# Performance work log

Measured on AMD Instinct MI355X. Metric: run time of the kernel, lower is better.

The kernel has to match this reference:

```python
import jax, jax.numpy as jnp
import numpy as np
from jax.scipy.special import gammaln

REG = 0.1  # reg_param from __init__


def setup_inputs() -> dict:
    key = jax.random.key(0)
    k1, k2 = jax.random.split(key)
    D, C, S, Q = 512, 64, 16, 2048  # feature_dim, n_way, shots, n_query
    X_support = jax.random.normal(k1, (C * S, D), dtype=jnp.float32)
    # balanced class labels (equivalent to argmax of a one-hot y)
    labels = jnp.arange(C * S, dtype=jnp.int32) % C
    X_query = jax.random.normal(k2, (Q, D), dtype=jnp.float32)
    # learned parameters, initialized exactly as in the torch module
    m = jnp.zeros((1, D), dtype=jnp.float32)
    kappa = jnp.asarray(0.1, dtype=jnp.float32)
    nu = jnp.asarray(float(D), dtype=jnp.float32)
    triu_diag = jnp.ones((D,), dtype=jnp.float32)
    triu_lower = jnp.eye(D, dtype=jnp.float32)
    return {"X_support": X_support, "labels": labels, "X_query": X_query,
            "m": m, "kappa": kappa, "nu": nu,
            "triu_diag": triu_diag, "triu_lower": triu_lower, "n_classes": 64}


def _forward(X_support, X_query, m, kappa, nu, triu_diag, triu_lower, labels, n_classes):
    N, D = X_support.shape
    C = int(n_classes)
    S = N // C  # balanced episode: N_j == S for every class

    # lower_triu = diag(|triu_diag|) + triu_lower * strictly_lower_mask
    mask = jnp.tril(jnp.ones((D, D), dtype=X_support.dtype), -1)
    L = jnp.diag(jnp.abs(triu_diag)) + triu_lower * mask

    kap = jnp.abs(kappa) + 1e-6
    nu_ = jnp.clip(nu, D - 1 + 1e-6)

    # group support samples by class: [C, S, D] (stable sort keeps per-class order)
    order = jnp.argsort(labels)
    Xg = X_support[order].reshape(C, S, D)
    Xmean = Xg.mean(axis=1)  # [C, D]

    # posterior means mu_j = kappa/(kappa+N) m + N/(kappa+N) mean(X_j)
    mu = (kap / (kap + S)) * m + (S / (kap + S)) * Xmean  # [C, D]

    # sum_outer(X_j) as one batched GEMM instead of a per-row loop
    XtX = jnp.einsum('csd,cse->cde', Xg, Xg)  # [C, D, D]
    base = L @ L.T + kap * (m.T @ m)          # [D, D], shared across classes
    S_ns = base[None] + XtX - (kap + S) * jnp.einsum('cd,ce->cde', mu, mu)
    sigma = S_ns * ((kap + S + 1.0) / ((nu_ + S - D + 1.0) * (kap + S)))  # [C, D, D]

    eye = jnp.eye(D, dtype=sigma.dtype)
    sigma_inv = (1.0 - REG) * jnp.linalg.inv(sigma) + REG * eye  # regularize()

    common = nu_ + S + 1.0 - D  # scalar (equal shots per class)
    _, logdet = jnp.linalg.slogdet(sigma)  # [C]
    bias = (gammaln(0.5 * (common + D)) - gammaln(0.5 * common)
            - 0.5 * D * jnp.log(common) - 0.5 * logdet)  # [C]

    # batched Mahalanobis distances: replaces nested python loops in predict()
    diff = X_query[None, :, :] - mu[:, None, :]              # [C, Q, D]
    t = jnp.einsum('cqd,cde->cqe', diff, sigma_inv)          # [C, Q, D]
    dist = jnp.sum(t * diff, axis=-1)                        # [C, Q]

    logits = bias[:, None] - 0.5 * (common + D) * jnp.log1p(dist / common)
    return logits.T  # [Q, C]


def reference(X_support, labels, X_query, m, kappa, nu, triu_diag, triu_lower, n_classes):
    return _forward(X_support, X_query, m, kappa, nu, triu_diag, triu_lower,
                    labels, n_classes)
```

## Files before the change

### kernel.cpp

```cpp
#include <hip/hip_runtime.h>
#include <math.h>

#define DD    512
#define CNUM  64
#define SHOTS 16
#define NSUP  1024
#define QNQ   2048
#define REGP  0.1f
#define XKS   4

typedef __attribute__((ext_vector_type(8))) short short8;
typedef __attribute__((ext_vector_type(4))) float f32x4;

__device__ __forceinline__ unsigned short f2bf(float f) {
  unsigned int u = __float_as_uint(f);
  unsigned int r = (u + 0x7fffu + ((u >> 16) & 1u)) >> 16;
  return (unsigned short)r;
}
__device__ __forceinline__ float bf2f(unsigned short h) {
  return __uint_as_float((unsigned int)h << 16);
}

static constexpr size_t OFF_W     = 0;
static constexpr size_t OFF_MU    = OFF_W     + 512*512;
static constexpr size_t OFF_Y     = OFF_MU    + 64*512;
static constexpr size_t OFF_Z     = OFF_Y     + 3136*512;
static constexpr size_t OFF_WM    = OFF_Z     + 3136;
static constexpr size_t OFF_CONST = OFF_WM    + 512;
static constexpr size_t OFF_IDX   = OFF_CONST + 16;
static constexpr size_t OFF_RMAP  = OFF_IDX   + 1024;
static constexpr size_t OFF_ZG    = OFF_RMAP  + 1088;
static constexpr size_t OFF_VMU   = OFF_ZG    + 1088;
static constexpr size_t OFF_MUBMU = OFF_VMU   + 1088;
static constexpr size_t OFF_MUN   = OFF_MUBMU + 64;
static constexpr size_t OFF_MINV  = OFF_MUN   + 64;
static constexpr size_t OFF_BIAS  = OFF_MINV  + 64*289;
static constexpr size_t OFF_QNRM  = OFF_BIAS  + 64;
static constexpr size_t OFF_YN    = OFF_QNRM  + 2048;
static constexpr size_t OFF_XMU   = OFF_YN    + 2048;
static constexpr size_t OFF_RG    = OFF_XMU   + (size_t)XKS*2048*64;
static constexpr size_t OFF_P     = OFF_RG    + 1088*2048;
static constexpr size_t OFF_PX    = OFF_P     + 3136*512;
static constexpr size_t OFF_PW    = OFF_PX    + 3136*512;


__global__ __launch_bounds__(256) void f_init(const float* tdiag, const float* tlow,
    const float* kappa, const float* nu, const int* labels, const float* Xs,
    const float* Xq, const float* m, float* W, float* cst, int* idx,
    int* rowmap, float* mu, float* mun,
    unsigned short* PX, unsigned short* PW) {
  __shared__ float sh[2 * 64 * 68 + 32 * 33];
  __shared__ int sidx[SHOTS];
  int b = blockIdx.x, tid = threadIdx.x;
  if (b == 0) {
    if (tid == 0) {
      float kap = fabsf(kappa[0]) + 1e-6f;
      float nu_ = fmaxf(nu[0], (float)(DD - 1) + 1e-6f);
      float common = nu_ + (float)SHOTS + 1.0f - (float)DD;
      float scale = (kap + SHOTS + 1.0f) / ((nu_ + SHOTS - DD + 1.0f) * (kap + SHOTS));
      cst[0] = kap;
      cst[1] = scale;
      cst[2] = common;
      cst[3] = 0.5f * (common + DD);
      cst[4] = lgammaf(0.5f * (common + DD)) - lgammaf(0.5f * common)
               - 0.5f * (float)DD * logf(common);
      cst[5] = -(kap + SHOTS);
      cst[6] = kap / (kap + SHOTS);
      cst[7] = 1.0f / (kap + SHOTS);
      cst[8] = (float)DD * logf(scale);
      cst[9] = -1.0f / (kap + SHOTS);
    }
  } else if (b < 65) {
    int c = b - 1;
    if (tid < 64) {
      int lane = tid, cnt = 0;
      for (int i0 = 0; i0 < NSUP; i0 += 64) {
        int lab = labels[i0 + lane];
        unsigned long long mm = __ballot(lab == c);
        if (lab == c) {
          int pos = cnt + __popcll(mm & ((1ull << lane) - 1ull));
          if (pos < SHOTS) idx[c * SHOTS + pos] = i0 + lane;
        }
        cnt += __popcll(mm);
      }
    }
    __syncthreads();
    if (tid < 17)
      rowmap[c * 17 + tid] = (tid < SHOTS) ? (QNQ + idx[c * SHOTS + tid])
                                           : (QNQ + NSUP + c);
  } else if (b < 129) {
    int c = b - 65;
    if (tid < 64) {
      int lane = tid, cnt = 0;
      for (int i0 = 0; i0 < NSUP; i0 += 64) {
        int lab = labels[i0 + lane];
        unsigned long long mm = __ballot(lab == c);
        if (lab == c) {
          int pos = cnt + __popcll(mm & ((1ull << lane) - 1ull));
          if (pos < SHOTS) sidx[pos] = i0 + lane;
        }
        cnt += __popcll(mm);
      }
    }
    __syncthreads();
    float kap = fabsf(kappa[0]) + 1e-6f;
    float cm = kap / (kap + SHOTS), cx = 1.0f / (kap + SHOTS);
    float* red = sh;
    float acc = 0.0f;
    size_t prow = (size_t)(3072 + c) * 1024;
    for (int d = tid; d < DD; d += 256) {
      float s = 0.0f;
      for (int sh_ = 0; sh_ < SHOTS; sh_++)
        s += Xs[(size_t)sidx[sh_] * DD + d];
      float v = cm * m[d] + cx * s;
      mu[(size_t)c * DD + d] = v;
      unsigned short h = f2bf(v), l = f2bf(v - bf2f(h));
      PX[prow + d] = h;
      PX[prow + 512 + d] = l;
      acc += v * v;
    }
    red[tid] = acc;
    __syncthreads();
    for (int off = 128; off > 0; off >>= 1) {
      if (tid < off) red[tid] += red[tid + off];
      __syncthreads();
    }
    if (tid == 0) mun[c] = red[0];
  } else if (b < 137) {
    int jb = b - 129;
    float* Ld = sh;
    float* Wd = sh + 64 * 68;
    float* tsh = sh + 2 * 64 * 68;
    for (int t = tid; t < 4096; t += 256) {
      int r = t >> 6, c = t & 63;
      int gr = jb * 64 + r;
      float v = (r == c) ? fabsf(tdiag[gr])
              : (r > c ? tlow[(size_t)gr * DD + jb * 64 + c] : 0.0f);
      Ld[r * 68 + c] = v;
      Wd[r * 68 + c] = 0.0f;
    }
    __syncthreads();
    if (tid < 64) {
      int s = tid >> 4, t = tid & 15;
      int r0 = s * 16;
      #pragma unroll
      for (int i = 0; i < 16; i++) {
        float w = (i == t) ? 1.0f : 0.0f;
        #pragma unroll
        for (int k = 0; k < 16; k++)
          if (k < i) w -= Ld[(r0 + i) * 68 + r0 + k] * Wd[(r0 + k) * 68 + r0 + t];
        Wd[(r0 + i) * 68 + r0 + t] = w / Ld[(r0 + i) * 68 + r0 + i];
      }
    }
    __syncthreads();
    for (int g2 = 0; g2 < 2; g2++) {
      int r0 = g2 * 32 + 16, c0 = g2 * 32;
      int rr = tid >> 4, cc = tid & 15;
      float t_ = 0.0f;
      #pragma unroll
      for (int k = 0; k < 16; k++)
        t_ += Ld[(r0 + rr) * 68 + c0 + k] * Wd[(c0 + k) * 68 + c0 + cc];
      tsh[rr * 33 + cc] = t_;
      __syncthreads();
      float x = 0.0f;
      #pragma unroll
      for (int k = 0; k < 16; k++)
        x -= Wd[(r0 + rr) * 68 + r0 + k] * tsh[k * 33 + cc];
      Wd[(r0 + rr) * 68 + c0 + cc] = x;
      __syncthreads();
    }
    {
      int rr = tid >> 6, cc = tid & 63;
      #pragma unroll
      for (int p = 0; p < 4; p++) {
        int r = rr + p * 4, c = cc;
        if (c < 32) {
          float t_ = 0.0f;
          #pragma unroll
          for (int k = 0; k < 32; k++)
            t_ += Ld[(32 + r) * 68 + k] * Wd[k * 68 + c];
          tsh[r * 33 + c] = t_;
        } else {
          int c2 = c - 32;
          float t_ = 0.0f;
          #pragma unroll
          for (int k = 0; k < 32; k++)
            t_ += Ld[(32 + r + 16) * 68 + k] * Wd[k * 68 + c2];
          tsh[(r + 16) * 33 + c2] = t_;
        }
      }
      __syncthreads();
      #pragma unroll
      for (int p = 0; p < 4; p++) {
        int r = rr + p * 4, c = cc;
        int r2 = (c < 32) ? r : r + 16;
        int c2 = (c < 32) ? c : c - 32;
        float x = 0.0f;
        #pragma unroll
        for (int k = 0; k < 32; k++)
          x -= Wd[(32 + r2) * 68 + 32 + k] * tsh[k * 33 + c2];
        Wd[(32 + r2) * 68 + c2] = x;
      }
    }
    __syncthreads();
    float* Wblk = W + (size_t)(jb * 64) * DD + jb * 64;
    for (int t = tid; t < 4096; t += 256) {
      int r = t >> 6, c = t & 63;
      float v = Wd[r * 68 + c];
      Wblk[(size_t)r * DD + c] = v;
      unsigned short h = f2bf(v), l = f2bf(v - bf2f(h));
      size_t prow = (size_t)(jb * 64 + r) * 1024 + jb * 64 + c;
      PW[prow] = h;
      PW[prow + 512] = l;
    }
  } else {
    int r0 = (b - 137) * 4;
    int row = r0 + (tid >> 6), lane = tid & 63;
    const float* src = (row < QNQ) ? Xq + (size_t)row * DD
                                   : Xs + (size_t)(row - QNQ) * DD;
    size_t prow = (size_t)row * 1024;
    #pragma unroll
    for (int p = 0; p < 2; p++) {
      int col = lane * 8 + p * 4;
      float4 v = *(const float4*)(src + col);
      ushort4 hi, lo;
      hi.x = f2bf(v.x); lo.x = f2bf(v.x - bf2f(hi.x));
      hi.y = f2bf(v.y); lo.y = f2bf(v.y - bf2f(hi.y));
      hi.z = f2bf(v.z); lo.z = f2bf(v.z - bf2f(hi.z));
      hi.w = f2bf(v.w); lo.w = f2bf(v.w - bf2f(hi.w));
      *(ushort4*)(PX + prow + col) = hi;
      *(ushort4*)(PX + prow + 512 + col) = lo;
    }
  }
}

__device__ __forceinline__ void tile_stage(float* S, const float* __restrict__ G, int ldg) {
  int tid = threadIdx.x;
  #pragma unroll
  for (int p = 0; p < 4; p++) {
    int f4 = tid + 256 * p;
    int row = f4 >> 4, c4 = (f4 & 15) * 4;
    *(float4*)&S[row * 68 + c4] = *(const float4*)(G + (size_t)row * ldg + c4);
  }
}
__device__ __forceinline__ void tile_fma(float acc[4][4], const float* As, const float* Bs) {
  int tid = threadIdx.x, tr = tid >> 4, tc = tid & 15;
  #pragma unroll
  for (int kk = 0; kk < 64; kk++) {
    float a[4];
    #pragma unroll
    for (int x = 0; x < 4; x++) a[x] = As[(tr * 4 + x) * 68 + kk];
    float4 bv = *(const float4*)&Bs[kk * 68 + tc * 4];
    float bb[4] = {bv.x, bv.y, bv.z, bv.w};
    #pragma unroll
    for (int x = 0; x < 4; x++)
      #pragma unroll
      for (int y = 0; y < 4; y++) acc[x][y] += a[x] * bb[y];
  }
}
__device__ __forceinline__ void tile_out_neg(const float acc[4][4], float* W,
    unsigned short* PW, int gr0, int gc0) {
  int tid = threadIdx.x, tr = tid >> 4, tc = tid & 15;
  #pragma unroll
  for (int x = 0; x < 4; x++) {
    #pragma unroll
    for (int y = 0; y < 4; y++) {
      float v = -acc[x][y];
      W[(size_t)(gr0 + tr * 4 + x) * DD + gc0 + tc * 4 + y] = v;
      unsigned short h = f2bf(v), l = f2bf(v - bf2f(h));
      size_t prow = (size_t)(gr0 + tr * 4 + x) * 1024 + gc0 + tc * 4 + y;
      PW[prow] = h;
      PW[prow + 512] = l;
    }
  }
}

#define GBK 16
__global__ __launch_bounds__(256) void k_m128_xmu(const float* __restrict__ tlow,
    const float* __restrict__ W_, float* __restrict__ Wout,
    const float* __restrict__ Xq, const float* __restrict__ Mu,
    float* __restrict__ xmup, unsigned short* __restrict__ PW) {
  __shared__ float sh[3 * 64 * 68];
  int b = blockIdx.x, tid = threadIdx.x;
  if (b < 4) {
    float* As = sh;
    float* Bs = sh + 64 * 68;
    float* tsh = sh + 2 * 64 * 68;
    int base = b * 128;
    float tacc[4][4] = {};
    tile_stage(As, tlow + (size_t)(base + 64) * DD + base, DD);
    tile_stage(Bs, W_ + (size_t)base * DD + base, DD);
    __syncthreads();
    tile_fma(tacc, As, Bs);
    __syncthreads();
    {
      int tr = tid >> 4, tc = tid & 15;
      #pragma unroll
      for (int x = 0; x < 4; x++)
        #pragma unroll
        for (int y = 0; y < 4; y++) tsh[(tr * 4 + x) * 68 + tc * 4 + y] = tacc[x][y];
    }
    tile_stage(As, W_ + (size_t)(base + 64) * DD + base + 64, DD);
    __syncthreads();
    float xacc[4][4] = {};
    tile_fma(xacc, As, tsh);
    tile_out_neg(xacc, Wout, PW, base + 64, base);
  } else {
    float* Ms = sh;
    float* Qs = sh + 64 * 68;
    int xb = b - 4;
    int bm = (xb & 63) * 32, kq = xb >> 6;
    int tr = tid >> 4, tc = tid & 15;
    float acc[4][2] = {};
    int k0s = kq * (DD / XKS), k0e = k0s + DD / XKS;
    for (int k0 = k0s; k0 < k0e; k0 += GBK) {
      {
        int row = tid >> 2, k4 = tid & 3;
        float4 v = *(const float4*)(Mu + (size_t)row * DD + k0 + k4 * 4);
        Ms[(k4 * 4 + 0) * 68 + row] = v.x; Ms[(k4 * 4 + 1) * 68 + row] = v.y;
        Ms[(k4 * 4 + 2) * 68 + row] = v.z; Ms[(k4 * 4 + 3) * 68 + row] = v.w;
      }
      if (tid < 128) {
        int row = tid >> 2, k4 = tid & 3;
        float4 v = *(const float4*)(Xq + (size_t)(bm + row) * DD + k0 + k4 * 4);
        Qs[(k4 * 4 + 0) * 36 + row] = v.x; Qs[(k4 * 4 + 1) * 36 + row] = v.y;
        Qs[(k4 * 4 + 2) * 36 + row] = v.z; Qs[(k4 * 4 + 3) * 36 + row] = v.w;
      }
      __syncthreads();
      #pragma unroll
      for (int kk = 0; kk < GBK; kk++) {
        float4 m0 = *(const float4*)&Ms[kk * 68 + tr * 4];
        float a[4] = {m0.x, m0.y, m0.z, m0.w};
        float q0 = Qs[kk * 36 + tc * 2], q1 = Qs[kk * 36 + tc * 2 + 1];
        #pragma unroll
        for (int y = 0; y < 4; y++) {
          acc[y][0] += a[y] * q0;
          acc[y][1] += a[y] * q1;
        }
      }
      __syncthreads();
    }
    #pragma unroll
    for (int y = 0; y < 4; y++) {
      float2 v = make_float2(acc[y][0], acc[y][1]);
      *(float2*)(xmup + ((size_t)kq * CNUM + tr * 4 + y) * QNQ + bm + tc * 2) = v;
    }
  }
}

__global__ __launch_bounds__(256) void k_m256(const float* __restrict__ tlow,
    float* __restrict__ W, unsigned short* __restrict__ PW) {
  __shared__ float sh[3 * 64 * 68];
  float* As = sh;
  float* Bs = sh + 64 * 68;
  float* tsh = sh + 2 * 64 * 68;
  int b = blockIdx.x, tid = threadIdx.x;
  int g = b >> 2, rem = b & 3, i = rem >> 1, j = rem & 1;
  int base = g * 256;
  float xacc[4][4] = {};
  for (int k = 0; k <= i; k++) {
    float tacc[4][4] = {};
    for (int l = j; l < 2; l++) {
      __syncthreads();
      tile_stage(As, tlow + (size_t)(base + 128 + 64 * k) * DD + base + 64 * l, DD);
      tile_stage(Bs, W + (size_t)(base + 64 * l) * DD + base + 64 * j, DD);
      __syncthreads();
      tile_fma(tacc, As, Bs);
    }
    __syncthreads();
    {
      int tr = tid >> 4, tc = tid & 15;
      #pragma unroll
      for (int x = 0; x < 4; x++)
        #pragma unroll
        for (int y = 0; y < 4; y++) tsh[(tr * 4 + x) * 68 + tc * 4 + y] = tacc[x][y];
    }
    tile_stage(As, W + (size_t)(base + 128 + 64 * i) * DD + base + 128 + 64 * k, DD);
    __syncthreads();
    tile_fma(xacc, As, tsh);
  }
  tile_out_neg(xacc, W, PW, base + 128 + 64 * i, base + 64 * j);
}

__device__ __forceinline__ void nn64_sh(float* As, float* Bs,
    const float* __restrict__ A, int lda, const float* __restrict__ B, int ldb,
    float* __restrict__ Cd, int ldc, int k0, int k1, float sgn,
    unsigned short* __restrict__ Pw, int gr0, int gc0) {
  int tid = threadIdx.x, tr = tid >> 4, tc = tid & 15;
  float acc[4][4] = {};
  for (int kc = k0; kc < k1; kc += 64) {
    #pragma unroll
    for (int p = 0; p < 4; p++) {
      int f4 = tid + 256 * p;
      int row = f4 >> 4, c4 = f4 & 15;
      *(float4*)&As[row * 68 + c4 * 4] = *(const float4*)(A + (size_t)row * lda + kc + c4 * 4);
      *(float4*)&Bs[row * 68 + c4 * 4] = *(const float4*)(B + (size_t)(kc + row) * ldb + c4 * 4);
    }
    __syncthreads();
    #pragma unroll
    for (int kk = 0; kk < 64; kk++) {
      float a[4];
      #pragma unroll
      for (int x = 0; x < 4; x++) a[x] = As[(tr * 4 + x) * 68 + kk];
      float4 bv = *(const float4*)&Bs[kk * 68 + tc * 4];
      float bb[4] = {bv.x, bv.y, bv.z, bv.w};
      #pragma unroll
      for (int x = 0; x < 4; x++)
        #pragma unroll
        for (int y = 0; y < 4; y++) acc[x][y] += a[x] * bb[y];
    }
    __syncthreads();
  }
  #pragma unroll
  for (int x = 0; x < 4; x++) {
    float4 v = make_float4(sgn * acc[x][0], sgn * acc[x][1],
                           sgn * acc[x][2], sgn * acc[x][3]);
    *(float4*)(Cd + (size_t)(tr * 4 + x) * ldc + tc * 4) = v;
    if (Pw) {
      size_t prow = (size_t)(gr0 + tr * 4 + x) * 1024 + gc0 + tc * 4;
      float vv[4] = {v.x, v.y, v.z, v.w};
      #pragma unroll
      for (int y = 0; y < 4; y++) {
        unsigned short h = f2bf(vv[y]), l = f2bf(vv[y] - bf2f(h));
        Pw[prow + y] = h;
        Pw[prow + 512 + y] = l;
      }
    }
  }
}

__global__ __launch_bounds__(256) void k_triT(const float* __restrict__ tlow,
                                              const float* __restrict__ W,
                                              float* __restrict__ T, int s) {
  __shared__ float sh[2 * 64 * 68];
  int h = s >> 1, tiles = h >> 6, per = tiles * tiles;
  int g = blockIdx.x / per, rem = blockIdx.x % per;
  int ti = rem / tiles, tj = rem % tiles;
  int base = g * s;
  const float* A = tlow + (size_t)(base + h + ti * 64) * DD + base;
  const float* B = W + (size_t)base * DD + base + tj * 64;
  float* Cd = T + (size_t)g * h * h + (size_t)(ti * 64) * h + tj * 64;
  nn64_sh(sh, sh + 64 * 68, A, DD, B, DD, Cd, h, tj * 64, h, 1.0f, nullptr, 0, 0);
}

__global__ __launch_bounds__(256) void k_triX(float* __restrict__ W,
                                              const float* __restrict__ T, int s,
                                              unsigned short* __restrict__ PW) {
  __shared__ float sh[2 * 64 * 68];
  int h = s >> 1, tiles = h >> 6, per = tiles * tiles;
  int g = blockIdx.x / per, rem = blockIdx.x % per;
  int ti = rem / tiles, tj = rem % tiles;
  int base = g * s;
  const float* A = W + (size_t)(base + h + ti * 64) * DD + base + h;
  const float* B = T + (size_t)g * h * h + tj * 64;
  int gr0 = base + h + ti * 64, gc0 = base + tj * 64;
  float* Cd = W + (size_t)gr0 * DD + gc0;
  nn64_sh(sh, sh + 64 * 68, A, DD, B, h, Cd, DD, 0, (ti + 1) * 64, -1.0f, PW, gr0, gc0);
}

#define PSTR 80
__global__ __launch_bounds__(256) void f_y_wm(const unsigned short* __restrict__ PX,
    const unsigned short* __restrict__ PW, const float* __restrict__ W,
    const float* __restrict__ m, float* __restrict__ Y,
    unsigned short* __restrict__ Pm, float* __restrict__ wm) {
  __shared__ unsigned short AshH[64 * PSTR];
  __shared__ unsigned short AshL[64 * PSTR];
  __shared__ unsigned short BshH[64 * PSTR];
  __shared__ unsigned short BshL[64 * PSTR];
  int b = blockIdx.x, tid = threadIdx.x;
  if (b < 392) {
    int mt = b >> 3, nt = b & 7;
    int bm = mt * 64, bn = nt * 64;
    int lane = tid & 63, wave = tid >> 6;
    int wr = wave >> 1, wc = wave & 1;
    int mrow = lane & 15, q = lane >> 4;
    f32x4 acc00 = {}, acc01 = {}, acc10 = {}, acc11 = {};
    int kchunks = nt + 1;
    for (int it = 0; it < kchunks; it++) {
      int kc = it * 64;
      #pragma unroll
      for (int p = 0; p < 2; p++) {
        int idx = tid + 256 * p;
        int row = idx >> 3, c8 = (idx & 7) * 8;
        *(short8*)&AshH[row * PSTR + c8] =
            *(const short8*)(PX + (size_t)(bm + row) * 1024 + kc + c8);
        *(short8*)&AshL[row * PSTR + c8] =
            *(const short8*)(PX + (size_t)(bm + row) * 1024 + 512 + kc + c8);
        *(short8*)&BshH[row * PSTR + c8] =
            *(const short8*)(PW + (size_t)(bn + row) * 1024 + kc + c8);
        *(short8*)&BshL[row * PSTR + c8] =
            *(const short8*)(PW + (size_t)(bn + row) * 1024 + 512 + kc + c8);
      }
      __syncthreads();
      #pragma unroll
      for (int ks = 0; ks < 2; ks++) {
        int ko = ks * 32 + q * 8;
        short8 ah0 = *(const short8*)&AshH[(wr * 32 + mrow) * PSTR + ko];
        short8 ah1 = *(const short8*)&AshH[(wr * 32 + 16 + mrow) * PSTR + ko];
        short8 al0 = *(const short8*)&AshL[(wr * 32 + mrow) * PSTR + ko];
        short8 al1 = *(const short8*)&AshL[(wr * 32 + 16 + mrow) * PSTR + ko];
        short8 bh0 = *(const short8*)&BshH[(wc * 32 + mrow) * PSTR + ko];
        short8 bh1 = *(const short8*)&BshH[(wc * 32 + 16 + mrow) * PSTR + ko];
        short8 bl0 = *(const short8*)&BshL[(wc * 32 + mrow) * PSTR + ko];
        short8 bl1 = *(const short8*)&BshL[(wc * 32 + 16 + mrow) * PSTR + ko];
        acc00 = __builtin_amdgcn_mfma_f32_16x16x32_bf16(ah0, bh0, acc00, 0, 0, 0);
        acc00 = __builtin_amdgcn_mfma_f32_16x16x32_bf16(ah0, bl0, acc00, 0, 0, 0);
        acc00 = __builtin_amdgcn_mfma_f32_16x16x32_bf16(al0, bh0, acc00, 0, 0, 0);
        acc00 = __builtin_amdgcn_mfma_f32_16x16x32_bf16(al0, bl0, acc00, 0, 0, 0);
        acc01 = __builtin_amdgcn_mfma_f32_16x16x32_bf16(ah0, bh1, acc01, 0, 0, 0);
        acc01 = __builtin_amdgcn_mfma_f32_16x16x32_bf16(ah0, bl1, acc01, 0, 0, 0);
        acc01 = __builtin_amdgcn_mfma_f32_16x16x32_bf16(al0, bh1, acc01, 0, 0, 0);
        acc01 = __builtin_amdgcn_mfma_f32_16x16x32_bf16(al0, bl1, acc01, 0, 0, 0);
        acc10 = __builtin_amdgcn_mfma_f32_16x16x32_bf16(ah1, bh0, acc10, 0, 0, 0);
        acc10 = __builtin_amdgcn_mfma_f32_16x16x32_bf16(ah1, bl0, acc10, 0, 0, 0);
        acc10 = __builtin_amdgcn_mfma_f32_16x16x32_bf16(al1, bh0, acc10, 0, 0, 0);
        acc10 = __builtin_amdgcn_mfma_f32_16x16x32_bf16(al1, bl0, acc10, 0, 0, 0);
        acc11 = __builtin_amdgcn_mfma_f32_16x16x32_bf16(ah1, bh1, acc11, 0, 0, 0);
        acc11 = __builtin_amdgcn_mfma_f32_16x16x32_bf16(ah1, bl1, acc11, 0, 0, 0);
        acc11 = __builtin_amdgcn_mfma_f32_16x16x32_bf16(al1, bh1, acc11, 0, 0, 0);
        acc11 = __builtin_amdgcn_mfma_f32_16x16x32_bf16(al1, bl1, acc11, 0, 0, 0);
      }
      __syncthreads();
    }
    #pragma unroll
    for (int r = 0; r < 4; r++) {
      int row0 = bm + wr * 32 + q * 4 + r;
      int row1 = row0 + 16;
      int col0 = bn + wc * 32 + mrow;
      float vv[4] = {acc00[r], acc01[r], acc10[r], acc11[r]};
      int rows[4] = {row0, row0, row1, row1};
      int cols[4] = {col0, col0 + 16, col0, col0 + 16};
      #pragma unroll
      for (int e = 0; e < 4; e++) {
        Y[(size_t)rows[e] * DD + cols[e]] = vv[e];
        unsigned short h = f2bf(vv[e]), l = f2bf(vv[e] - bf2f(h));
        Pm[(size_t)rows[e] * 1024 + cols[e]] = h;
        Pm[(size_t)rows[e] * 1024 + 512 + cols[e]] = l;
      }
    }
  } else {
    int wave = tid >> 6, lane = tid & 63;
    int row = (b - 392) * 4 + wave;
    float s = 0.0f;
    for (int j = lane; j <= row; j += 64) s += W[(size_t)row * DD + j] * m[j];
    for (int off = 32; off > 0; off >>= 1) s += __shfl_down(s, off);
    if (lane == 0) wm[row] = s;
  }
}

__global__ __launch_bounds__(256) void f_z_rg_gram(const unsigned short* __restrict__ Pm,
    const float* __restrict__ Y, const float* __restrict__ tdiag,
    const int* __restrict__ rowmap, const float* __restrict__ Xq,
    const float* __restrict__ wm, float* __restrict__ cst,
    float* __restrict__ Rg,
    float* __restrict__ z, float* __restrict__ qn, float* __restrict__ yn,
    float* __restrict__ zg, float* __restrict__ Vmu, float* __restrict__ muBmu,
    float* __restrict__ Minv, float* __restrict__ bias) {
  __shared__ float sh[9920];
  __shared__ float csmS;
  int b = blockIdx.x, tid = threadIdx.x;
  if (b < 64) {
    int c = b;
    int lane = tid & 63, wave = tid >> 6;
    float* Ys  = sh;
    float* aug = sh + 8772;
    float* zsv = aug + 306;
    float kap = cst[0], cst9 = cst[9];
    for (int t = tid; t < 17 * 128; t += 256) {
      int r = t >> 7, col = t & 127;
      *(float4*)&Ys[r * 516 + col * 4] =
          *(const float4*)(Y + (size_t)rowmap[c * 17 + r] * DD + col * 4);
    }
    float ldb_r = 0.0f;
    if (wave == 0) {
      float aa = 0.0f, ll = 0.0f;
      for (int t = lane; t < DD; t += 64) {
        float w = wm[t]; aa += w * w;
        ll += logf(fabsf(tdiag[t]));
      }
      #pragma unroll
      for (int off = 32; off > 0; off >>= 1) {
        aa += __shfl_xor(aa, off);
        ll += __shfl_xor(ll, off);
      }
      ldb_r = 2.0f * ll + logf(1.0f + kap * aa);
      if (lane == 0) csmS = kap / (1.0f + kap * aa);
    }
    __syncthreads();
    if (wave > 0) {
      for (int a = wave - 1; a < 17; a += 3) {
        float s = 0.0f;
        for (int j = lane; j < 128; j += 64) {
          float4 yv = *(const float4*)&Ys[a * 516 + j * 4];
          float4 wv = *(const float4*)(wm + j * 4);
          s += yv.x * wv.x + yv.y * wv.y + yv.z * wv.z + yv.w * wv.w;
        }
        #pragma unroll
        for (int off = 32; off > 0; off >>= 1) s += __shfl_xor(s, off);
        if (lane == 0) zsv[a] = s;
      }
    }
    __syncthreads();
    float csm = csmS;
    for (int e = tid; e < 153; e += 256) {
      int a = (int)((sqrtf(8.0f * (float)e + 1.0f) - 1.0f) * 0.5f);
      while (((a + 1) * (a + 2)) / 2 <= e) a++;
      while ((a * (a + 1)) / 2 > e) a--;
      int bb = e - (a * (a + 1)) / 2;
      const float* ra = &Ys[a * 516];
      const float* rb = &Ys[bb * 516];
      float s = 0.0f;
      for (int k = 0; k < 128; k++) {
        float4 va = *(const float4*)&ra[k * 4];
        float4 vb = *(const float4*)&rb[k * 4];
        s += va.x * vb.x + va.y * vb.y + va.z * vb.z + va.w * vb.w;
      }
      float g = s - csm * zsv[a] * zsv[bb];
      if (a == bb) g += (a < 16) ? 1.0f : cst9;
      aug[a * 18 + bb] = g;
      if (a != bb) aug[bb * 18 + a] = g;
    }
    __syncthreads();
    if (wave == 0) {
      float colv[17];
      bool left = lane < 17;
      bool right = (lane >= 17 && lane < 34);
      #pragma unroll
      for (int r = 0; r < 17; r++) {
        float lv = aug[r * 18 + (lane & 31)];
        colv[r] = left ? lv : ((right && (lane - 17) == r) ? 1.0f : 0.0f);
      }
      float det = 0.0f;
      #pragma unroll
      for (int k = 0; k < 17; k++) {
        float best = fabsf(colv[k]); int bp = k;
        #pragma unroll
        for (int r = k + 1; r < 17; r++) {
          float v = fabsf(colv[r]);
          if (v > best) { best = v; bp = r; }
        }
        int p = __shfl(bp, k);
        float pv = colv[k];
        #pragma unroll
        for (int r = k + 1; r < 17; r++) pv = (p == r) ? colv[r] : pv;
        float oldk = colv[k];
        #pragma unroll
        for (int r = k + 1; r < 17; r++) colv[r] = (p == r) ? oldk : colv[r];
        colv[k] = pv;
        float piv = __shfl(pv, k);
        if (lane == 0) det += logf(fabsf(piv));
        float invp = 1.0f / piv;
        float rk = pv * invp;
        colv[k] = rk;
        #pragma unroll
        for (int r = 0; r < 17; r++) {
          if (r == k) continue;
          float ck = __shfl(colv[r], k);
          colv[r] = fmaf(-ck, rk, colv[r]);
        }
      }
      if (right) {
        int bb = lane - 17;
        #pragma unroll
        for (int r = 0; r < 17; r++)
          Minv[(size_t)c * 289 + r * 17 + bb] = colv[r];
      }
      if (lane == 0) {
        float slog = logf(fabsf(cst[5])) + det;
        float logdetSigma = cst[8] + ldb_r + slog;
        bias[c] = cst[4] - 0.5f * logdetSigma;
      }
    } else if (wave == 1) {
      if (lane < 17) {
        float gv = aug[lane * 18 + 16];
        if (lane == 16) gv -= cst9;
        Vmu[c * 17 + lane] = gv;
        if (lane == 16) muBmu[c] = gv;
        zg[c * 17 + lane] = zsv[lane];
      }
    }
  } else if (b == 64) {
    if (tid < 64) {
      float aa = 0.0f, ll = 0.0f;
      for (int t = tid; t < DD; t += 64) {
        float w = wm[t]; aa += w * w;
        ll += logf(fabsf(tdiag[t]));
      }
      #pragma unroll
      for (int off = 32; off > 0; off >>= 1) {
        aa += __shfl_xor(aa, off);
        ll += __shfl_xor(ll, off);
      }
      if (tid == 0) {
        float kap = cst[0];
        cst[10] = kap / (1.0f + kap * aa);
        cst[11] = 2.0f * ll + logf(1.0f + kap * aa);
      }
    }
  } else if (b < 609) {
    unsigned short* ush = (unsigned short*)sh;
    unsigned short* Ash = ush;
    unsigned short* Bsh = ush + 64 * PSTR;
    unsigned short* Csh = ush + 2 * 64 * PSTR;
    int rb = b - 65;
    int bm = (rb >> 5) * 64, bn = (rb & 31) * 64;
    int lane = tid & 63, wave = tid >> 6;
    int wr = wave >> 1, wc = wave & 1;
    int mrow = lane & 15, q = lane >> 4;
    int srowA[2];
    #pragma unroll
    for (int p = 0; p < 2; p++) srowA[p] = rowmap[bm + ((tid + 256 * p) >> 3)];
    f32x4 acc00 = {}, acc01 = {}, acc10 = {}, acc11 = {};
    for (int it = 0; it < 16; it++) {
      int kc = it * 64;
      int kcX = kc ^ 512;
      #pragma unroll
      for (int p = 0; p < 2; p++) {
        int idx = tid + 256 * p;
        int row = idx >> 3, c8 = (idx & 7) * 8;
        *(short8*)&Ash[row * PSTR + c8] =
            *(const short8*)(Pm + (size_t)srowA[p] * 1024 + kc + c8);
        *(short8*)&Bsh[row * PSTR + c8] =
            *(const short8*)(Pm + (size_t)(bn + row) * 1024 + kc + c8);
        *(short8*)&Csh[row * PSTR + c8] =
            *(const short8*)(Pm + (size_t)(bn + row) * 1024 + kcX + c8);
      }
      __syncthreads();
      #pragma unroll
      for (int ks = 0; ks < 2; ks++) {
        int ko = ks * 32 + q * 8;
        short8 a0 = *(const short8*)&Ash[(wr * 32 + mrow) * PSTR + ko];
        short8 a1 = *(const short8*)&Ash[(wr * 32 + 16 + mrow) * PSTR + ko];
        short8 b0 = *(const short8*)&Bsh[(wc * 32 + mrow) * PSTR + ko];
        short8 b1 = *(const short8*)&Bsh[(wc * 32 + 16 + mrow) * PSTR + ko];
        short8 c0 = *(const short8*)&Csh[(wc * 32 + mrow) * PSTR + ko];
        short8 c1 = *(const short8*)&Csh[(wc * 32 + 16 + mrow) * PSTR + ko];
        acc00 = __builtin_amdgcn_mfma_f32_16x16x32_bf16(a0, b0, acc00, 0, 0, 0);
        acc01 = __builtin_amdgcn_mfma_f32_16x16x32_bf16(a0, b1, acc01, 0, 0, 0);
        acc10 = __builtin_amdgcn_mfma_f32_16x16x32_bf16(a1, b0, acc10, 0, 0, 0);
        acc11 = __builtin_amdgcn_mfma_f32_16x16x32_bf16(a1, b1, acc11, 0, 0, 0);
        acc00 = __builtin_amdgcn_mfma_f32_16x16x32_bf16(a0, c0, acc00, 0, 0, 0);
        acc01 = __builtin_amdgcn_mfma_f32_16x16x32_bf16(a0, c1, acc01, 0, 0, 0);
        acc10 = __builtin_amdgcn_mfma_f32_16x16x32_bf16(a1, c0, acc10, 0, 0, 0);
        acc11 = __builtin_amdgcn_mfma_f32_16x16x32_bf16(a1, c1, acc11, 0, 0, 0);
      }
      __syncthreads();
    }
    #pragma unroll
    for (int r = 0; r < 4; r++) {
      int row0 = bm + wr * 32 + q * 4 + r;
      int row1 = row0 + 16;
      int col0 = bn + wc * 32 + mrow;
      Rg[(size_t)row0 * QNQ + col0]      = acc00[r];
      Rg[(size_t)row0 * QNQ + col0 + 16] = acc01[r];
      Rg[(size_t)row1 * QNQ + col0]      = acc10[r];
      Rg[(size_t)row1 * QNQ + col0 + 16] = acc11[r];
    }
  } else {
    int wave = tid >> 6, lane = tid & 63;
    int row = (b - 609) * 4 + wave;
    const float* xr = Xq + (size_t)row * DD;
    const float* yr = Y + (size_t)row * DD;
    float sz = 0.0f, s1 = 0.0f, s2 = 0.0f;
    for (int j4 = lane; j4 < 128; j4 += 64) {
      float4 xv = *(const float4*)(xr + j4 * 4);
      float4 yv = *(const float4*)(yr + j4 * 4);
      float4 wv = *(const float4*)(wm + j4 * 4);
      sz += yv.x * wv.x + yv.y * wv.y + yv.z * wv.z + yv.w * wv.w;
      s1 += xv.x * xv.x + xv.y * xv.y + xv.z * xv.z + xv.w * xv.w;
      s2 += yv.x * yv.x + yv.y * yv.y + yv.z * yv.z + yv.w * yv.w;
    }
    for (int off = 32; off > 0; off >>= 1) {
      sz += __shfl_down(sz, off);
      s1 += __shfl_down(s1, off);
      s2 += __shfl_down(s2, off);
    }
    if (lane == 0) {
      z[row] = sz;
      qn[row] = s1;
      yn[row] = s2;
    }
  }
}

__global__ __launch_bounds__(256) void k_logits(const float* __restrict__ Rg,
    const float* z, const float* zg,
    const float* Vmu, const float* muBmu, const float* mun, const float* yn,
    const float* qn, const float* xmup, const float* Minv, const float* bias,
    const float* cst, float* out) {
  __shared__ float Ms[289], Vs[17], Zs[17];
  int c = blockIdx.y;
  int q = blockIdx.x * 256 + threadIdx.x;
  for (int t = threadIdx.x; t < 289; t += 256) Ms[t] = Minv[(size_t)c * 289 + t];
  if (threadIdx.x < 17) {
    Vs[threadIdx.x] = Vmu[c * 17 + threadIdx.x];
    Zs[threadIdx.x] = zg[c * 17 + threadIdx.x];
  }
  __syncthreads();
  float csm = cst[10], scale = cst[1], common = cst[2], coef = cst[3];
  float zq = z[q];
  float r[17];
  float xBmu = 0.0f;
  for (int a = 0; a < 17; a++) {
    float raw = Rg[(size_t)(c * 17 + a) * QNQ + q] - csm * Zs[a] * zq;
    if (a == 16) xBmu = raw;
    r[a] = raw - Vs[a];
  }
  float qB = yn[q] - csm * zq * zq;
  float quadB = qB - 2.0f * xBmu + muBmu[c];
  float corr = 0.0f;
  for (int a = 0; a < 17; a++) {
    float e = 0.0f;
    for (int bb = 0; bb < 17; bb++) e += Ms[a * 17 + bb] * r[bb];
    corr += r[a] * e;
  }
  float distB = (quadB - corr) / scale;
  float xm = 0.0f;
  #pragma unroll
  for (int p = 0; p < XKS; p++)
    xm += xmup[((size_t)(p * CNUM + c)) * QNQ + q];
  float dn = qn[q] - 2.0f * xm + mun[c];
  float dist = (1.0f - REGP) * distB + REGP * dn;
  out[(size_t)q * CNUM + c] = bias[c] - coef * log1pf(dist / common);
}

extern "C" void kernel_launch(void* const* d_in, const int* in_sizes, int n_in,
                              void* d_out, int out_size, void* d_ws, size_t ws_size,
                              hipStream_t stream) {
  const float* Xs    = (const float*)d_in[0];
  const int*   labels= (const int*)d_in[1];
  const float* Xq    = (const float*)d_in[2];
  const float* m     = (const float*)d_in[3];
  const float* kappa = (const float*)d_in[4];
  const float* nu    = (const float*)d_in[5];
  const float* tdiag = (const float*)d_in[6];
  const float* tlow  = (const float*)d_in[7];
  float* ws = (float*)d_ws;
  float* W    = ws + OFF_W;
  float* mu   = ws + OFF_MU;
  float* Y    = ws + OFF_Y;
  float* z    = ws + OFF_Z;
  float* wm   = ws + OFF_WM;
  float* cst  = ws + OFF_CONST;
  int*   idx  = (int*)(ws + OFF_IDX);
  int*   rmap = (int*)(ws + OFF_RMAP);
  float* zg   = ws + OFF_ZG;
  float* Vmu  = ws + OFF_VMU;
  float* muBmu= ws + OFF_MUBMU;
  float* mun  = ws + OFF_MUN;
  float* Minv = ws + OFF_MINV;
  float* bias = ws + OFF_BIAS;
  float* qn   = ws + OFF_QNRM;
  float* yn   = ws + OFF_YN;
  float* xmup = ws + OFF_XMU;
  float* Rg   = ws + OFF_RG;
  unsigned short* P  = (unsigned short*)(ws + OFF_P);
  unsigned short* PX = (unsigned short*)(ws + OFF_PX);
  unsigned short* PW = (unsigned short*)(ws + OFF_PW);
  float* Ttmp = ws + OFF_RG;
  float* out  = (float*)d_out;

  f_init<<<905, 256, 0, stream>>>(tdiag, tlow, kappa, nu, labels, Xs, Xq, m,
                                  W, cst, idx, rmap, mu, mun, PX, PW);
  k_m128_xmu<<<260, 256, 0, stream>>>(tlow, W, W, Xq, mu, xmup, PW);
  k_m256<<<8, 256, 0, stream>>>(tlow, W, PW);
  k_triT<<<16, 256, 0, stream>>>(tlow, W, Ttmp, 512);
  k_triX<<<16, 256, 0, stream>>>(W, Ttmp, 512, PW);
  f_y_wm<<<520, 256, 0, stream>>>(PX, PW, W, m, Y, P, wm);
  f_z_rg_gram<<<64 + 1 + 544 + 512, 256, 0, stream>>>(P, Y, tdiag, rmap, Xq, wm,
                                                      cst, Rg, z, qn, yn,
                                                      zg, Vmu, muBmu, Minv, bias);
  k_logits<<<dim3(QNQ / 256, CNUM), 256, 0, stream>>>(Rg, z, zg, Vmu, muBmu,
                                                      mun, yn, qn, xmup, Minv, bias,
                                                      cst, out);
  (void)in_sizes; (void)n_in; (void)out_size; (void)ws_size;
}
```

Measured before the change: 189.1 us.

## Spread bf16 split conversion across small kernels and drop lo*lo MFMA terms

Moves the fp32-to-bf16 hi/lo split of query and support rows out of the init kernel into spare blocks of the under-occupied triangular-solve kernels, so that work fills otherwise idle CUs. The triangular-solve blocks move to the front of the init grid so the slowest blocks start first. Both split-bf16 GEMMs now skip the low*low product, the gram GEMM is restructured from a K=1024 swapped-half loop to an explicit hi/lo 3-term loop, and the LDS padding stride is reduced. Dropping the lo*lo term slightly lowers precision.

```diff
diff --git a/kernel.cpp b/kernel.cpp
--- a/kernel.cpp
+++ b/kernel.cpp
@@ -44,6 +44,27 @@
 static constexpr size_t OFF_PW    = OFF_PX    + 3136*512;
 
 
+__device__ __forceinline__ void px_rows(const float* __restrict__ Xq,
+    const float* __restrict__ Xs, unsigned short* __restrict__ PX, int r0) {
+  int tid = threadIdx.x;
+  int row = r0 + (tid >> 6), lane = tid & 63;
+  const float* src = (row < QNQ) ? Xq + (size_t)row * DD
+                                 : Xs + (size_t)(row - QNQ) * DD;
+  size_t prow = (size_t)row * 1024;
+  #pragma unroll
+  for (int p = 0; p < 2; p++) {
+    int col = lane * 8 + p * 4;
+    float4 v = *(const float4*)(src + col);
+    ushort4 hi, lo;
+    hi.x = f2bf(v.x); lo.x = f2bf(v.x - bf2f(hi.x));
+    hi.y = f2bf(v.y); lo.y = f2bf(v.y - bf2f(hi.y));
+    hi.z = f2bf(v.z); lo.z = f2bf(v.z - bf2f(hi.z));
+    hi.w = f2bf(v.w); lo.w = f2bf(v.w - bf2f(hi.w));
+    *(ushort4*)(PX + prow + col) = hi;
+    *(ushort4*)(PX + prow + 512 + col) = lo;
+  }
+}
+
 __global__ __launch_bounds__(256) void f_init(const float* tdiag, const float* tlow,
     const float* kappa, const float* nu, const int* labels, const float* Xs,
     const float* Xq, const float* m, float* W, float* cst, int* idx,
@@ -52,7 +73,94 @@
   __shared__ float sh[2 * 64 * 68 + 32 * 33];
   __shared__ int sidx[SHOTS];
   int b = blockIdx.x, tid = threadIdx.x;
-  if (b == 0) {
+  if (b < 8) {
+    int jb = b;
+    float* Ld = sh;
+    float* Wd = sh + 64 * 68;
+    float* tsh = sh + 2 * 64 * 68;
+    for (int t = tid; t < 4096; t += 256) {
+      int r = t >> 6, c = t & 63;
+      int gr = jb * 64 + r;
+      float v = (r == c) ? fabsf(tdiag[gr])
+              : (r > c ? tlow[(size_t)gr * DD + jb * 64 + c] : 0.0f);
+      Ld[r * 68 + c] = v;
+      Wd[r * 68 + c] = 0.0f;
+    }
+    __syncthreads();
+    if (tid < 64) {
+      int s = tid >> 4, t = tid & 15;
+      int r0 = s * 16;
+      #pragma unroll
+      for (int i = 0; i < 16; i++) {
+        float w = (i == t) ? 1.0f : 0.0f;
+        #pragma unroll
+        for (int k = 0; k < 16; k++)
+          if (k < i) w -= Ld[(r0 + i) * 68 + r0 + k] * Wd[(r0 + k) * 68 + r0 + t];
+        Wd[(r0 + i) * 68 + r0 + t] = w / Ld[(r0 + i) * 68 + r0 + i];
+      }
+    }
+    __syncthreads();
+    for (int g2 = 0; g2 < 2; g2++) {
+      int r0 = g2 * 32 + 16, c0 = g2 * 32;
+      int rr = tid >> 4, cc = tid & 15;
+      float t_ = 0.0f;
+      #pragma unroll
+      for (int k = 0; k < 16; k++)
+        t_ += Ld[(r0 + rr) * 68 + c0 + k] * Wd[(c0 + k) * 68 + c0 + cc];
+      tsh[rr * 33 + cc] = t_;
+      __syncthreads();
+      float x = 0.0f;
+      #pragma unroll
+      for (int k = 0; k < 16; k++)
+        x -= Wd[(r0 + rr) * 68 + r0 + k] * tsh[k * 33 + cc];
+      Wd[(r0 + rr) * 68 + c0 + cc] = x;
+      __syncthreads();
+    }
+    {
+      int rr = tid >> 6, cc = tid & 63;
+      #pragma unroll
+      for (int p = 0; p < 4; p++) {
+        int r = rr + p * 4, c = cc;
+        if (c < 32) {
+          float t_ = 0.0f;
+          #pragma unroll
+          for (int k = 0; k < 32; k++)
+            t_ += Ld[(32 + r) * 68 + k] * Wd[k * 68 + c];
+          tsh[r * 33 + c] = t_;
+        } else {
+          int c2 = c - 32;
+          float t_ = 0.0f;
+          #pragma unroll
+          for (int k = 0; k < 32; k++)
+            t_ += Ld[(32 + r + 16) * 68 + k] * Wd[k * 68 + c2];
+          tsh[(r + 16) * 33 + c2] = t_;
+        }
+      }
+      __syncthreads();
+      #pragma unroll
+      for (int p = 0; p < 4; p++) {
+        int r = rr + p * 4, c = cc;
+        int r2 = (c < 32) ? r : r + 16;
+        int c2 = (c < 32) ? c : c - 32;
+        float x = 0.0f;
+        #pragma unroll
+        for (int k = 0; k < 32; k++)
+          x -= Wd[(32 + r2) * 68 + 32 + k] * tsh[k * 33 + c2];
+        Wd[(32 + r2) * 68 + c2] = x;
+      }
+    }
+    __syncthreads();
+    float* Wblk = W + (size_t)(jb * 64) * DD + jb * 64;
+    for (int t = tid; t < 4096; t += 256) {
+      int r = t >> 6, c = t & 63;
+      float v = Wd[r * 68 + c];
+      Wblk[(size_t)r * DD + c] = v;
+      unsigned short h = f2bf(v), l = f2bf(v - bf2f(h));
+      size_t prow = (size_t)(jb * 64 + r) * 1024 + jb * 64 + c;
+      PW[prow] = h;
+      PW[prow + 512] = l;
+    }
+  } else if (b == 8) {
     if (tid == 0) {
       float kap = fabsf(kappa[0]) + 1e-6f;
       float nu_ = fmaxf(nu[0], (float)(DD - 1) + 1e-6f);
@@ -70,8 +178,8 @@
       cst[8] = (float)DD * logf(scale);
       cst[9] = -1.0f / (kap + SHOTS);
     }
-  } else if (b < 65) {
-    int c = b - 1;
+  } else if (b < 73) {
+    int c = b - 9;
     if (tid < 64) {
       int lane = tid, cnt = 0;
       for (int i0 = 0; i0 < NSUP; i0 += 64) {
@@ -88,8 +196,8 @@
     if (tid < 17)
       rowmap[c * 17 + tid] = (tid < SHOTS) ? (QNQ + idx[c * SHOTS + tid])
                                            : (QNQ + NSUP + c);
-  } else if (b < 129) {
-    int c = b - 65;
+  } else {
+    int c = b - 73;
     if (tid < 64) {
       int lane = tid, cnt = 0;
       for (int i0 = 0; i0 < NSUP; i0 += 64) {
@@ -126,111 +234,6 @@
       __syncthreads();
     }
     if (tid == 0) mun[c] = red[0];
-  } else if (b < 137) {
-    int jb = b - 129;
-    float* Ld = sh;
-    float* Wd = sh + 64 * 68;
-    float* tsh = sh + 2 * 64 * 68;
-    for (int t = tid; t < 4096; t += 256) {
-      int r = t >> 6, c = t & 63;
-      int gr = jb * 64 + r;
-      float v = (r == c) ? fabsf(tdiag[gr])
-              : (r > c ? tlow[(size_t)gr * DD + jb * 64 + c] : 0.0f);
-      Ld[r * 68 + c] = v;
-      Wd[r * 68 + c] = 0.0f;
-    }
-    __syncthreads();
-    if (tid < 64) {
-      int s = tid >> 4, t = tid & 15;
-      int r0 = s * 16;
-      #pragma unroll
-      for (int i = 0; i < 16; i++) {
-        float w = (i == t) ? 1.0f : 0.0f;
-        #pragma unroll
-        for (int k = 0; k < 16; k++)
-          if (k < i) w -= Ld[(r0 + i) * 68 + r0 + k] * Wd[(r0 + k) * 68 + r0 + t];
-        Wd[(r0 + i) * 68 + r0 + t] = w / Ld[(r0 + i) * 68 + r0 + i];
-      }
-    }
-    __syncthreads();
-    for (int g2 = 0; g2 < 2; g2++) {
-      int r0 = g2 * 32 + 16, c0 = g2 * 32;
-      int rr = tid >> 4, cc = tid & 15;
-      float t_ = 0.0f;
-      #pragma unroll
-      for (int k = 0; k < 16; k++)
-        t_ += Ld[(r0 + rr) * 68 + c0 + k] * Wd[(c0 + k) * 68 + c0 + cc];
-      tsh[rr * 33 + cc] = t_;
-      __syncthreads();
-      float x = 0.0f;
-      #pragma unroll
-      for (int k = 0; k < 16; k++)
-        x -= Wd[(r0 + rr) * 68 + r0 + k] * tsh[k * 33 + cc];
-      Wd[(r0 + rr) * 68 + c0 + cc] = x;
-      __syncthreads();
-    }
-    {
-      int rr = tid >> 6, cc = tid & 63;
-      #pragma unroll
-      for (int p = 0; p < 4; p++) {
-        int r = rr + p * 4, c = cc;
-        if (c < 32) {
-          float t_ = 0.0f;
-          #pragma unroll
-          for (int k = 0; k < 32; k++)
-            t_ += Ld[(32 + r) * 68 + k] * Wd[k * 68 + c];
-          tsh[r * 33 + c] = t_;
-        } else {
-          int c2 = c - 32;
-          float t_ = 0.0f;
-          #pragma unroll
-          for (int k = 0; k < 32; k++)
-            t_ += Ld[(32 + r + 16) * 68 + k] * Wd[k * 68 + c2];
-          tsh[(r + 16) * 33 + c2] = t_;
-        }
-      }
-      __syncthreads();
-      #pragma unroll
-      for (int p = 0; p < 4; p++) {
-        int r = rr + p * 4, c = cc;
-        int r2 = (c < 32) ? r : r + 16;
-        int c2 = (c < 32) ? c : c - 32;
-        float x = 0.0f;
-        #pragma unroll
-        for (int k = 0; k < 32; k++)
-          x -= Wd[(32 + r2) * 68 + 32 + k] * tsh[k * 33 + c2];
-        Wd[(32 + r2) * 68 + c2] = x;
-      }
-    }
-    __syncthreads();
-    float* Wblk = W + (size_t)(jb * 64) * DD + jb * 64;
-    for (int t = tid; t < 4096; t += 256) {
-      int r = t >> 6, c = t & 63;
-      float v = Wd[r * 68 + c];
-      Wblk[(size_t)r * DD + c] = v;
-      unsigned short h = f2bf(v), l = f2bf(v - bf2f(h));
-      size_t prow = (size_t)(jb * 64 + r) * 1024 + jb * 64 + c;
-      PW[prow] = h;
-      PW[prow + 512] = l;
-    }
-  } else {
-    int r0 = (b - 137) * 4;
-    int row = r0 + (tid >> 6), lane = tid & 63;
-    const float* src = (row < QNQ) ? Xq + (size_t)row * DD
-                                   : Xs + (size_t)(row - QNQ) * DD;
-    size_t prow = (size_t)row * 1024;
-    #pragma unroll
-    for (int p = 0; p < 2; p++) {
-      int col = lane * 8 + p * 4;
-      float4 v = *(const float4*)(src + col);
-      ushort4 hi, lo;
-      hi.x = f2bf(v.x); lo.x = f2bf(v.x - bf2f(hi.x));
-      hi.y = f2bf(v.y); lo.y = f2bf(v.y - bf2f(hi.y));
-      hi.z = f2bf(v.z); lo.z = f2bf(v.z - bf2f(hi.z));
-      hi.w = f2bf(v.w); lo.w = f2bf(v.w - bf2f(hi.w));
-      *(ushort4*)(PX + prow + col) = hi;
-      *(ushort4*)(PX + prow + 512 + col) = lo;
-    }
   }
 }
 
@@ -349,12 +352,15 @@
 }
 
 __global__ __launch_bounds__(256) void k_m256(const float* __restrict__ tlow,
-    float* __restrict__ W, unsigned short* __restrict__ PW) {
+    float* __restrict__ W, unsigned short* __restrict__ PW,
+    const float* __restrict__ Xq, const float* __restrict__ Xs,
+    unsigned short* __restrict__ PX) {
   __shared__ float sh[3 * 64 * 68];
+  int b = blockIdx.x, tid = threadIdx.x;
+  if (b >= 8) { px_rows(Xq, Xs, PX, (b - 8) * 4); return; }
   float* As = sh;
   float* Bs = sh + 64 * 68;
   float* tsh = sh + 2 * 64 * 68;
-  int b = blockIdx.x, tid = threadIdx.x;
   int g = b >> 2, rem = b & 3, i = rem >> 1, j = rem & 1;
   int base = g * 256;
   float xacc[4][4] = {};
@@ -431,34 +437,38 @@
 
 __global__ __launch_bounds__(256) void k_triT(const float* __restrict__ tlow,
                                               const float* __restrict__ W,
-                                              float* __restrict__ T, int s) {
+                                              float* __restrict__ T,
+                                              const float* __restrict__ Xq,
+                                              const float* __restrict__ Xs,
+                                              unsigned short* __restrict__ PX) {
   __shared__ float sh[2 * 64 * 68];
-  int h = s >> 1, tiles = h >> 6, per = tiles * tiles;
-  int g = blockIdx.x / per, rem = blockIdx.x % per;
-  int ti = rem / tiles, tj = rem % tiles;
-  int base = g * s;
-  const float* A = tlow + (size_t)(base + h + ti * 64) * DD + base;
-  const float* B = W + (size_t)base * DD + base + tj * 64;
-  float* Cd = T + (size_t)g * h * h + (size_t)(ti * 64) * h + tj * 64;
-  nn64_sh(sh, sh + 64 * 68, A, DD, B, DD, Cd, h, tj * 64, h, 1.0f, nullptr, 0, 0);
+  int b = blockIdx.x;
+  if (b >= 16) { px_rows(Xq, Xs, PX, 1024 + (b - 16) * 4); return; }
+  int ti = b >> 2, tj = b & 3;
+  const float* A = tlow + (size_t)(256 + ti * 64) * DD;
+  const float* B = W + (size_t)tj * 64;
+  float* Cd = T + (size_t)(ti * 64) * 256 + tj * 64;
+  nn64_sh(sh, sh + 64 * 68, A, DD, B, DD, Cd, 256, tj * 64, 256, 1.0f, nullptr, 0, 0);
 }
 
 __global__ __launch_bounds__(256) void k_triX(float* __restrict__ W,
-                                              const float* __restrict__ T, int s,
-                                              unsigned short* __restrict__ PW) {
+                                              const float* __restrict__ T,
+                                              unsigned short* __restrict__ PW,
+                                              const float* __restrict__ Xq,
+                                              const float* __restrict__ Xs,
+                                              unsigned short* __restrict__ PX) {
   __shared__ float sh[2 * 64 * 68];
-  int h = s >> 1, tiles = h >> 6, per = tiles * tiles;
-  int g = blockIdx.x / per, rem = blockIdx.x % per;
-  int ti = rem / tiles, tj = rem % tiles;
-  int base = g * s;
-  const float* A = W + (size_t)(base + h + ti * 64) * DD + base + h;
-  const float* B = T + (size_t)g * h * h + tj * 64;
-  int gr0 = base + h + ti * 64, gc0 = base + tj * 64;
+  int b = blockIdx.x;
+  if (b >= 16) { px_rows(Xq, Xs, PX, 2048 + (b - 16) * 4); return; }
+  int ti = b >> 2, tj = b & 3;
+  const float* A = W + (size_t)(256 + ti * 64) * DD + 256;
+  const float* B = T + tj * 64;
+  int gr0 = 256 + ti * 64, gc0 = tj * 64;
   float* Cd = W + (size_t)gr0 * DD + gc0;
-  nn64_sh(sh, sh + 64 * 68, A, DD, B, h, Cd, DD, 0, (ti + 1) * 64, -1.0f, PW, gr0, gc0);
-}
-
-#define PSTR 80
+  nn64_sh(sh, sh + 64 * 68, A, DD, B, 256, Cd, DD, 0, (ti + 1) * 64, -1.0f, PW, gr0, gc0);
+}
+
+#define PSTR 72
 __global__ __launch_bounds__(256) void f_y_wm(const unsigned short* __restrict__ PX,
     const unsigned short* __restrict__ PW, const float* __restrict__ W,
     const float* __restrict__ m, float* __restrict__ Y,
@@ -506,19 +516,15 @@
         acc00 = __builtin_amdgcn_mfma_f32_16x16x32_bf16(ah0, bh0, acc00, 0, 0, 0);
         acc00 = __builtin_amdgcn_mfma_f32_16x16x32_bf16(ah0, bl0, acc00, 0, 0, 0);
         acc00 = __builtin_amdgcn_mfma_f32_16x16x32_bf16(al0, bh0, acc00, 0, 0, 0);
-        acc00 = __builtin_amdgcn_mfma_f32_16x16x32_bf16(al0, bl0, acc00, 0, 0, 0);
         acc01 = __builtin_amdgcn_mfma_f32_16x16x32_bf16(ah0, bh1, acc01, 0, 0, 0);
         acc01 = __builtin_amdgcn_mfma_f32_16x16x32_bf16(ah0, bl1, acc01, 0, 0, 0);
         acc01 = __builtin_amdgcn_mfma_f32_16x16x32_bf16(al0, bh1, acc01, 0, 0, 0);
-        acc01 = __builtin_amdgcn_mfma_f32_16x16x32_bf16(al0, bl1, acc01, 0, 0, 0);
         acc10 = __builtin_amdgcn_mfma_f32_16x16x32_bf16(ah1, bh0, acc10, 0, 0, 0);
         acc10 = __builtin_amdgcn_mfma_f32_16x16x32_bf16(ah1, bl0, acc10, 0, 0, 0);
         acc10 = __builtin_amdgcn_mfma_f32_16x16x32_bf16(al1, bh0, acc10, 0, 0, 0);
-        acc10 = __builtin_amdgcn_mfma_f32_16x16x32_bf16(al1, bl0, acc10, 0, 0, 0);
         acc11 = __builtin_amdgcn_mfma_f32_16x16x32_bf16(ah1, bh1, acc11, 0, 0, 0);
         acc11 = __builtin_amdgcn_mfma_f32_16x16x32_bf16(ah1, bl1, acc11, 0, 0, 0);
         acc11 = __builtin_amdgcn_mfma_f32_16x16x32_bf16(al1, bh1, acc11, 0, 0, 0);
-        acc11 = __builtin_amdgcn_mfma_f32_16x16x32_bf16(al1, bl1, acc11, 0, 0, 0);
       }
       __syncthreads();
     }
@@ -556,7 +562,7 @@
     float* __restrict__ z, float* __restrict__ qn, float* __restrict__ yn,
     float* __restrict__ zg, float* __restrict__ Vmu, float* __restrict__ muBmu,
     float* __restrict__ Minv, float* __restrict__ bias) {
-  __shared__ float sh[9920];
+  __shared__ float sh[9216];
   __shared__ float csmS;
   int b = blockIdx.x, tid = threadIdx.x;
   if (b < 64) {
@@ -699,9 +705,10 @@
     }
   } else if (b < 609) {
     unsigned short* ush = (unsigned short*)sh;
-    unsigned short* Ash = ush;
-    unsigned short* Bsh = ush + 64 * PSTR;
-    unsigned short* Csh = ush + 2 * 64 * PSTR;
+    unsigned short* AH = ush;
+    unsigned short* AL = ush + 64 * PSTR;
+    unsigned short* BH = ush + 2 * 64 * PSTR;
+    unsigned short* BL = ush + 3 * 64 * PSTR;
     int rb = b - 65;
     int bm = (rb >> 5) * 64, bn = (rb & 31) * 64;
     int lane = tid & 63, wave = tid >> 6;
@@ -711,38 +718,45 @@
     #pragma unroll
     for (int p = 0; p < 2; p++) srowA[p] = rowmap[bm + ((tid + 256 * p) >> 3)];
     f32x4 acc00 = {}, acc01 = {}, acc10 = {}, acc11 = {};
-    for (int it = 0; it < 16; it++) {
+    for (int it = 0; it < 8; it++) {
       int kc = it * 64;
-      int kcX = kc ^ 512;
       #pragma unroll
       for (int p = 0; p < 2; p++) {
         int idx = tid + 256 * p;
         int row = idx >> 3, c8 = (idx & 7) * 8;
-        *(short8*)&Ash[row * PSTR + c8] =
+        *(short8*)&AH[row * PSTR + c8] =
             *(const short8*)(Pm + (size_t)srowA[p] * 1024 + kc + c8);
-        *(short8*)&Bsh[row * PSTR + c8] =
+        *(short8*)&AL[row * PSTR + c8] =
+            *(const short8*)(Pm + (size_t)srowA[p] * 1024 + 512 + kc + c8);
+        *(short8*)&BH[row * PSTR + c8] =
             *(const short8*)(Pm + (size_t)(bn + row) * 1024 + kc + c8);
-        *(short8*)&Csh[row * PSTR + c8] =
-            *(const short8*)(Pm + (size_t)(bn + row) * 1024 + kcX + c8);
+        *(short8*)&BL[row * PSTR + c8] =
+            *(const short8*)(Pm + (size_t)(bn + row) * 1024 + 512 + kc + c8);
       }
       __syncthreads();
       #pragma unroll
       for (int ks = 0; ks < 2; ks++) {
         int ko = ks * 32 + q * 8;
-        short8 a0 = *(const short8*)&Ash[(wr * 32 + mrow) * PSTR + ko];
-        short8 a1 = *(const short8*)&Ash[(wr * 32 + 16 + mrow) * PSTR + ko];
-        short8 b0 = *(const short8*)&Bsh[(wc * 32 + mrow) * PSTR + ko];
-        short8 b1 = *(const short8*)&Bsh[(wc * 32 + 16 + mrow) * PSTR + ko];
-        short8 c0 = *(const short8*)&Csh[(wc * 32 + mrow) * PSTR + ko];
-        short8 c1 = *(const short8*)&Csh[(wc * 32 + 16 + mrow) * PSTR + ko];
-        acc00 = __builtin_amdgcn_mfma_f32_16x16x32_bf16(a0, b0, acc00, 0, 0, 0);
-        acc01 = __builtin_amdgcn_mfma_f32_16x16x32_bf16(a0, b1, acc01, 0, 0, 0);
-        acc10 = __builtin_amdgcn_mfma_f32_16x16x32_bf16(a1, b0, acc10, 0, 0, 0);
-        acc11 = __builtin_amdgcn_mfma_f32_16x16x32_bf16(a1, b1, acc11, 0, 0, 0);
-        acc00 = __builtin_amdgcn_mfma_f32_16x16x32_bf16(a0, c0, acc00, 0, 0, 0);
-        acc01 = __builtin_amdgcn_mfma_f32_16x16x32_bf16(a0, c1, acc01, 0, 0, 0);
-        acc10 = __builtin_amdgcn_mfma_f32_16x16x32_bf16(a1, c0, acc10, 0, 0, 0);
-        acc11 = __builtin_amdgcn_mfma_f32_16x16x32_bf16(a1, c1, acc11, 0, 0, 0);
+        short8 ah0 = *(const short8*)&AH[(wr * 32 + mrow) * PSTR + ko];
+        short8 ah1 = *(const short8*)&AH[(wr * 32 + 16 + mrow) * PSTR + ko];
+        short8 al0 = *(const short8*)&AL[(wr * 32 + mrow) * PSTR + ko];
+        short8 al1 = *(const short8*)&AL[(wr * 32 + 16 + mrow) * PSTR + ko];
+        short8 bh0 = *(const short8*)&BH[(wc * 32 + mrow) * PSTR + ko];
+        short8 bh1 = *(const short8*)&BH[(wc * 32 + 16 + mrow) * PSTR + ko];
+        short8 bl0 = *(const short8*)&BL[(wc * 32 + mrow) * PSTR + ko];
+        short8 bl1 = *(const short8*)&BL[(wc * 32 + 16 + mrow) * PSTR + ko];
+        acc00 = __builtin_amdgcn_mfma_f32_16x16x32_bf16(ah0, bh0, acc00, 0, 0, 0);
+        acc00 = __builtin_amdgcn_mfma_f32_16x16x32_bf16(ah0, bl0, acc00, 0, 0, 0);
+        acc00 = __builtin_amdgcn_mfma_f32_16x16x32_bf16(al0, bh0, acc00, 0, 0, 0);
+        acc01 = __builtin_amdgcn_mfma_f32_16x16x32_bf16(ah0, bh1, acc01, 0, 0, 0);
+        acc01 = __builtin_amdgcn_mfma_f32_16x16x32_bf16(ah0, bl1, acc01, 0, 0, 0);
+        acc01 = __builtin_amdgcn_mfma_f32_16x16x32_bf16(al0, bh1, acc01, 0, 0, 0);
+        acc10 = __builtin_amdgcn_mfma_f32_16x16x32_bf16(ah1, bh0, acc10, 0, 0, 0);
+        acc10 = __builtin_amdgcn_mfma_f32_16x16x32_bf16(ah1, bl0, acc10, 0, 0, 0);
+        acc10 = __builtin_amdgcn_mfma_f32_16x16x32_bf16(al1, bh0, acc10, 0, 0, 0);
+        acc11 = __builtin_amdgcn_mfma_f32_16x16x32_bf16(ah1, bh1, acc11, 0, 0, 0);
+        acc11 = __builtin_amdgcn_mfma_f32_16x16x32_bf16(ah1, bl1, acc11, 0, 0, 0);
+        acc11 = __builtin_amdgcn_mfma_f32_16x16x32_bf16(al1, bh1, acc11, 0, 0, 0);
       }
       __syncthreads();
     }
@@ -860,12 +874,12 @@
   float* Ttmp = ws + OFF_RG;
   float* out  = (float*)d_out;
 
-  f_init<<<905, 256, 0, stream>>>(tdiag, tlow, kappa, nu, labels, Xs, Xq, m,
+  f_init<<<137, 256, 0, stream>>>(tdiag, tlow, kappa, nu, labels, Xs, Xq, m,
                                   W, cst, idx, rmap, mu, mun, PX, PW);
   k_m128_xmu<<<260, 256, 0, stream>>>(tlow, W, W, Xq, mu, xmup, PW);
-  k_m256<<<8, 256, 0, stream>>>(tlow, W, PW);
-  k_triT<<<16, 256, 0, stream>>>(tlow, W, Ttmp, 512);
-  k_triX<<<16, 256, 0, stream>>>(W, Ttmp, 512, PW);
+  k_m256<<<8 + 256, 256, 0, stream>>>(tlow, W, PW, Xq, Xs, PX);
+  k_triT<<<16 + 256, 256, 0, stream>>>(tlow, W, Ttmp, Xq, Xs, PX);
+  k_triX<<<16 + 256, 256, 0, stream>>>(W, Ttmp, PW, Xq, Xs, PX);
   f_y_wm<<<520, 256, 0, stream>>>(PX, PW, W, m, Y, P, wm);
   f_z_rg_gram<<<64 + 1 + 544 + 512, 256, 0, stream>>>(P, Y, tdiag, rmap, Xq, wm,
                                                       cst, Rg, z, qn, yn,
```

After: 187.5 us. About the same (-0.8%).
